# Optimization experiments

Measured on AMD Instinct MI355X. Metric: run time of the kernel, lower is better.

The kernel has to match this reference:

```python
import jax, jax.numpy as jnp
import numpy as np

N_EMBD = 1024
EXPAND = 2
D_INNER = N_EMBD * EXPAND          # 2048
D_STATE = 64
N_HEADS = D_INNER // D_STATE       # 32
HEAD_DIM = D_INNER // N_HEADS      # 64
N_GROUPS = 1
D_CONV = 4
N_LAYERS = 48
BATCH, SEQ = 1, 512
PROJ_SIZE = 2 * D_INNER + N_HEADS + 2 * N_GROUPS * D_STATE  # 4256
EPS = 1e-6


def setup_inputs() -> dict:
    key = jax.random.key(0)
    ks = jax.random.split(key, 6)
    init_std = 0.02
    proj_std = 0.02 / np.sqrt(2 * N_LAYERS)
    return {
        "x": jax.random.normal(ks[0], (BATCH, SEQ, N_EMBD), jnp.float32),
        "norm_scale": jnp.ones((N_EMBD,), jnp.float32),
        "w_in": jax.random.normal(ks[1], (N_EMBD, PROJ_SIZE), jnp.float32) * init_std,
        "conv_weight": jax.random.normal(ks[2], (D_CONV, D_INNER), jnp.float32) * 0.02,
        "conv_bias": jnp.zeros((D_INNER,), jnp.float32),
        "A_log": jnp.log(0.5 + jnp.arange(N_HEADS, dtype=jnp.float32) * 0.5 / N_HEADS),
        "dt_bias": jax.random.normal(ks[3], (N_HEADS,), jnp.float32) * 0.1,
        "w_out": jax.random.normal(ks[4], (D_INNER, N_EMBD), jnp.float32) * proj_std,
    }


def _mamba_fwd(x, norm_scale, w_in, conv_weight, conv_bias, A_log, dt_bias, w_out):
    b, T, _ = x.shape
    residual = x
    # RMSNorm
    xn = x * jax.lax.rsqrt(jnp.mean(x * x, axis=-1, keepdims=True) + EPS) * norm_scale
    # in_proj and split
    proj = xn @ w_in  # (b, T, proj_size)
    gate = proj[..., :D_INNER]
    ssm_in = proj[..., D_INNER:2 * D_INNER]
    dt_raw = proj[..., 2 * D_INNER:2 * D_INNER + N_HEADS]
    gs = N_GROUPS * D_STATE
    B = proj[..., 2 * D_INNER + N_HEADS:2 * D_INNER + N_HEADS + gs].reshape(b, T, N_GROUPS, D_STATE)
    C = proj[..., 2 * D_INNER + N_HEADS + gs:].reshape(b, T, N_GROUPS, D_STATE)
    # causal depthwise short conv (cross-correlation, matching lax.conv semantics)
    xp = jnp.pad(ssm_in, ((0, 0), (D_CONV - 1, 0), (0, 0)))
    conv = conv_bias + sum(conv_weight[k] * xp[:, k:k + T, :] for k in range(D_CONV))
    h = jax.nn.silu(conv)  # (b, T, d_inner)
    dt = jax.nn.softplus(dt_raw + dt_bias)  # (b, T, H)
    A = -jnp.exp(A_log)  # (H,)
    A_bar = jnp.exp(A[None, None, :] * dt)  # (b, T, H)
    # heads / groups
    hpg = N_HEADS // N_GROUPS
    xh = h.reshape(b, T, N_HEADS, HEAD_DIM)
    Bh = jnp.repeat(B, hpg, axis=2)  # (b, T, H, N)
    Ch = jnp.repeat(C, hpg, axis=2)  # (b, T, H, N)
    # Bu[b,t,h,p,n] = B[b,t,h,n] * dt[b,t,h] * x[b,t,h,p]
    Bu = Bh[:, :, :, None, :] * (dt[..., None, None] * xh[..., None])  # (b,T,H,P,N)

    def _binary_op(left, right):
        a_l, b_l = left
        a_r, b_r = right
        return (a_l * a_r, a_r * b_l + b_r)

    # A_bar broadcast to (b,T,H,1,1) so the pair broadcasts against Bu
    _, states = jax.lax.associative_scan(_binary_op, (A_bar[..., None, None], Bu), axis=1)
    y = jnp.einsum('bthpn,bthn->bthp', states, Ch).reshape(b, T, D_INNER)
    y = y * jax.nn.silu(gate)
    y = y @ w_out
    return residual + y


def reference(x, norm_scale, w_in, conv_weight, conv_bias, A_log, dt_bias, w_out):
    return _mamba_fwd(x, norm_scale, w_in, conv_weight, conv_bias, A_log, dt_bias, w_out)
```

## Files before the change

### kernel.cpp

```cpp
#include <hip/hip_runtime.h>
#include <hip/hip_bf16.h>

typedef unsigned short u16;
typedef float f32x4v __attribute__((ext_vector_type(4)));
typedef short short8 __attribute__((ext_vector_type(8)));

#define TSEQ 512
#define EMB  1024
#define DI   2048
#define NH   32
#define DS   64
#define PROJ 4256
#define PROJP 4352
#define NCH  8
#define LCH  64
#define KSPLIT2 4

__device__ __forceinline__ u16 f2bf(float f) {
    union { __hip_bfloat16 h; u16 u; } cv;
    cv.h = __float2bfloat16(f);
    return cv.u;
}
__device__ __forceinline__ unsigned pack2(float a, float b) {
    return (unsigned)f2bf(a) | ((unsigned)f2bf(b) << 16);
}

__global__ __launch_bounds__(256) void k_transpose_cast(
        const float* __restrict__ src, u16* __restrict__ dst, int K, int N) {
    __shared__ float tile[64][65];
    const int n0 = blockIdx.x * 64;
    const int k0 = blockIdx.y * 64;
    const int tid = threadIdx.x;
    const int c  = tid & 63;
    const int r4 = tid >> 6;
    #pragma unroll
    for (int i = 0; i < 16; ++i) {
        int r = r4 + i * 4;
        float v = 0.f;
        if (n0 + c < N) v = src[(size_t)(k0 + r) * N + n0 + c];
        tile[r][c] = v;
    }
    __syncthreads();
    const int rk = tid & 63;
    const int cn = tid >> 6;
    #pragma unroll
    for (int i = 0; i < 16; ++i) {
        int n = cn + i * 4;
        dst[(size_t)(n0 + n) * K + k0 + rk] = f2bf(tile[rk][n]);
    }
}

__global__ __launch_bounds__(256) void k_rmsnorm(
        const float* __restrict__ x, const float* __restrict__ scale,
        u16* __restrict__ xnb) {
    const int t = blockIdx.x, tid = threadIdx.x;
    const float4* xr = (const float4*)(x + (size_t)t * EMB);
    float4 v = xr[tid];
    float ss = v.x * v.x + v.y * v.y + v.z * v.z + v.w * v.w;
    #pragma unroll
    for (int off = 32; off; off >>= 1) ss += __shfl_xor(ss, off);
    __shared__ float ws4[4];
    if ((tid & 63) == 0) ws4[tid >> 6] = ss;
    __syncthreads();
    float tot = ws4[0] + ws4[1] + ws4[2] + ws4[3];
    float inv = rsqrtf(tot * (1.f / EMB) + 1e-6f);
    float4 s = ((const float4*)scale)[tid];
    uint2 o;
    o.x = pack2(v.x * inv * s.x, v.y * inv * s.y);
    o.y = pack2(v.z * inv * s.z, v.w * inv * s.w);
    ((uint2*)xnb)[(size_t)t * 256 + tid] = o;
}

template<int BM, int BN>
__global__ __launch_bounds__(256) void k_gemm(
        const u16* __restrict__ A, int lda,
        const u16* __restrict__ BT, int ldb,
        float* __restrict__ C, int ldc, int Kper) {
    constexpr int WM = BM / 2, WN = BN / 2, FM = WM / 16, FN = WN / 16;
    constexpr int NA = BM * 8 / 256, NB = BN * 8 / 256;
    __shared__ __align__(16) u16 Al[BM][72];
    __shared__ __align__(16) u16 Bl[BN][72];
    const int tid = threadIdx.x;
    const int wid = tid >> 6, lane = tid & 63;
    const int wr = wid >> 1, wc = wid & 1;
    const int ar = lane & 15, kg = lane >> 4;
    const int row0 = blockIdx.y * BM, col0 = blockIdx.x * BN;
    const int kbase = blockIdx.z * Kper;
    const int Mtot = gridDim.y * BM;
    float* Cz = C + (size_t)blockIdx.z * Mtot * ldc;

    short8 ra[NA], rb[NB];
    auto load_stage = [&](int k0) {
        #pragma unroll
        for (int j = 0; j < NA; ++j) {
            int idx = tid + j * 256;
            ra[j] = *(const short8*)(A + (size_t)(row0 + (idx >> 3)) * lda + k0 + (idx & 7) * 8);
        }
        #pragma unroll
        for (int j = 0; j < NB; ++j) {
            int idx = tid + j * 256;
            rb[j] = *(const short8*)(BT + (size_t)(col0 + (idx >> 3)) * ldb + k0 + (idx & 7) * 8);
        }
    };
    auto write_stage = [&]() {
        #pragma unroll
        for (int j = 0; j < NA; ++j) {
            int idx = tid + j * 256;
            *(short8*)&Al[idx >> 3][(idx & 7) * 8] = ra[j];
        }
        #pragma unroll
        for (int j = 0; j < NB; ++j) {
            int idx = tid + j * 256;
            *(short8*)&Bl[idx >> 3][(idx & 7) * 8] = rb[j];
        }
    };

    f32x4v acc[FM][FN] = {};
    const int NT = Kper / 64;
    load_stage(kbase);
    for (int kt = 0; kt < NT; ++kt) {
        write_stage();
        __syncthreads();
        if (kt + 1 < NT) load_stage(kbase + (kt + 1) * 64);
        #pragma unroll
        for (int kk = 0; kk < 2; ++kk) {
            short8 af[FM], bf[FN];
            #pragma unroll
            for (int m = 0; m < FM; ++m)
                af[m] = *(const short8*)&Al[wr * WM + m * 16 + ar][kk * 32 + kg * 8];
            #pragma unroll
            for (int n = 0; n < FN; ++n)
                bf[n] = *(const short8*)&Bl[wc * WN + n * 16 + ar][kk * 32 + kg * 8];
            #pragma unroll
            for (int m = 0; m < FM; ++m)
                #pragma unroll
                for (int n = 0; n < FN; ++n)
                    acc[m][n] = __builtin_amdgcn_mfma_f32_16x16x32_bf16(
                        af[m], bf[n], acc[m][n], 0, 0, 0);
        }
        __syncthreads();
    }
    #pragma unroll
    for (int m = 0; m < FM; ++m)
        #pragma unroll
        for (int n = 0; n < FN; ++n)
            #pragma unroll
            for (int j = 0; j < 4; ++j) {
                int row = row0 + wr * WM + m * 16 + kg * 4 + j;
                int col = col0 + wc * WN + n * 16 + ar;
                Cz[(size_t)row * ldc + col] = acc[m][n][j];
            }
}

__global__ __launch_bounds__(256) void k_reduce_out(
        const float* __restrict__ part, const float* __restrict__ x,
        float* __restrict__ out) {
    int i = blockIdx.x * 256 + threadIdx.x;
    float4 v = ((const float4*)x)[i];
    #pragma unroll
    for (int z = 0; z < KSPLIT2; ++z) {
        float4 p = ((const float4*)part)[(size_t)z * (TSEQ * EMB / 4) + i];
        v.x += p.x; v.y += p.y; v.z += p.z; v.w += p.w;
    }
    ((float4*)out)[i] = v;
}

__global__ __launch_bounds__(256) void k_dt(
        const float* __restrict__ proj, const float* __restrict__ A_log,
        const float* __restrict__ dt_bias, float* __restrict__ dtw,
        float* __restrict__ abw) {
    int idx = blockIdx.x * 256 + threadIdx.x;
    int t = idx >> 5, hh = idx & 31;
    float z = proj[(size_t)t * PROJP + 2 * DI + hh] + dt_bias[hh];
    float dt = (z > 20.f) ? z : log1pf(expf(z));
    float ab = expf(-expf(A_log[hh]) * dt);
    dtw[idx] = dt;
    abw[idx] = ab;
}

__global__ __launch_bounds__(256) void k_conv(
        const float* __restrict__ proj, const float* __restrict__ cw,
        const float* __restrict__ cb, float* __restrict__ hout) {
    int idx = blockIdx.x * 256 + threadIdx.x;
    int t = idx >> 11, c = idx & 2047;
    float acc = cb[c];
    #pragma unroll
    for (int k = 0; k < 4; ++k) {
        int tt = t + k - 3;
        if (tt >= 0) acc += cw[k * DI + c] * proj[(size_t)tt * PROJP + DI + c];
    }
    hout[idx] = acc / (1.f + expf(-acc));
}

__global__ __launch_bounds__(256) void k_scan1(
        const float* __restrict__ proj, const float* __restrict__ hconv,
        const float* __restrict__ dtw, const float* __restrict__ abw,
        float* __restrict__ Sloc, float* __restrict__ Pc) {
    const int c = blockIdx.x, h = blockIdx.y;
    const int tid = threadIdx.x;
    const int q = tid & 3, p = tid >> 2, n0 = q * 16;
    __shared__ __align__(16) float Blds[64][64];
    __shared__ __align__(16) float xl[64][64];
    __shared__ float al[64], dl[64];
    for (int i = tid; i < 4096; i += 256) {
        int t = i >> 6, n = i & 63;
        Blds[t][n] = proj[(size_t)(c * 64 + t) * PROJP + 2 * DI + NH + n];
        xl[t][n]   = hconv[(size_t)(c * 64 + t) * DI + h * 64 + n];
    }
    if (tid < 64) {
        al[tid] = abw[(c * 64 + tid) * NH + h];
        dl[tid] = dtw[(c * 64 + tid) * NH + h];
    }
    __syncthreads();
    float s[16] = {0.f,0.f,0.f,0.f,0.f,0.f,0.f,0.f,0.f,0.f,0.f,0.f,0.f,0.f,0.f,0.f};
    for (int t = 0; t < 64; ++t) {
        float a = al[t];
        float dtx = dl[t] * xl[t][p];
        const float4* brow = (const float4*)&Blds[t][n0];
        #pragma unroll
        for (int i4 = 0; i4 < 4; ++i4) {
            float4 b = brow[i4];
            s[i4*4+0] = a * s[i4*4+0] + dtx * b.x;
            s[i4*4+1] = a * s[i4*4+1] + dtx * b.y;
            s[i4*4+2] = a * s[i4*4+2] + dtx * b.z;
            s[i4*4+3] = a * s[i4*4+3] + dtx * b.w;
        }
    }
    float* dst = Sloc + ((size_t)(c * 32 + h) * 64 + p) * 64 + n0;
    #pragma unroll
    for (int i4 = 0; i4 < 4; ++i4)
        ((float4*)dst)[i4] = make_float4(s[i4*4], s[i4*4+1], s[i4*4+2], s[i4*4+3]);
    if (tid == 0) {
        float pr = 1.f;
        for (int t = 0; t < 64; ++t) pr *= al[t];
        Pc[c * 32 + h] = pr;
    }
}

__global__ __launch_bounds__(256) void k_scan2(
        const float* __restrict__ Sloc, const float* __restrict__ Pc,
        float* __restrict__ Sinit) {
    int gid = blockIdx.x * 256 + threadIdx.x;
    int h = gid >> 12, rem = gid & 4095;
    float s = 0.f;
    #pragma unroll
    for (int c = 0; c < NCH; ++c) {
        size_t o = (size_t)(c * 32 + h) * 4096 + rem;
        Sinit[o] = s;
        s = Pc[c * 32 + h] * s + Sloc[o];
    }
}

__global__ __launch_bounds__(256) void k_scan3(
        const float* __restrict__ proj, const float* __restrict__ hconv,
        const float* __restrict__ dtw, const float* __restrict__ abw,
        const float* __restrict__ Sinit, u16* __restrict__ yg) {
    const int c = blockIdx.x, h = blockIdx.y;
    const int tid = threadIdx.x;
    const int q = tid & 3, p = tid >> 2, n0 = q * 16;
    __shared__ __align__(16) float Blds[64][64];
    __shared__ __align__(16) float Clds[64][64];
    __shared__ __align__(16) float xl[64][64];
    __shared__ float al[64], dl[64];
    for (int i = tid; i < 4096; i += 256) {
        int t = i >> 6, n = i & 63;
        Blds[t][n] = proj[(size_t)(c * 64 + t) * PROJP + 2 * DI + NH + n];
        Clds[t][n] = proj[(size_t)(c * 64 + t) * PROJP + 2 * DI + NH + DS + n];
        xl[t][n]   = hconv[(size_t)(c * 64 + t) * DI + h * 64 + n];
    }
    if (tid < 64) {
        al[tid] = abw[(c * 64 + tid) * NH + h];
        dl[tid] = dtw[(c * 64 + tid) * NH + h];
    }
    __syncthreads();
    float s[16];
    const float* si = Sinit + ((size_t)(c * 32 + h) * 64 + p) * 64 + n0;
    #pragma unroll
    for (int i4 = 0; i4 < 4; ++i4) {
        float4 v = ((const float4*)si)[i4];
        s[i4*4+0] = v.x; s[i4*4+1] = v.y; s[i4*4+2] = v.z; s[i4*4+3] = v.w;
    }
    for (int t = 0; t < 64; ++t) {
        float a = al[t];
        float dtx = dl[t] * xl[t][p];
        const float4* brow = (const float4*)&Blds[t][n0];
        const float4* crow = (const float4*)&Clds[t][n0];
        float yp = 0.f;
        #pragma unroll
        for (int i4 = 0; i4 < 4; ++i4) {
            float4 b = brow[i4], cc = crow[i4];
            s[i4*4+0] = a * s[i4*4+0] + dtx * b.x; yp += s[i4*4+0] * cc.x;
            s[i4*4+1] = a * s[i4*4+1] + dtx * b.y; yp += s[i4*4+1] * cc.y;
            s[i4*4+2] = a * s[i4*4+2] + dtx * b.z; yp += s[i4*4+2] * cc.z;
            s[i4*4+3] = a * s[i4*4+3] + dtx * b.w; yp += s[i4*4+3] * cc.w;
        }
        yp += __shfl_xor(yp, 1);
        yp += __shfl_xor(yp, 2);
        if (q == 0) xl[t][p] = yp;
    }
    __syncthreads();
    for (int i = tid; i < 4096; i += 256) {
        int t = i >> 6, pp = i & 63;
        float y = xl[t][pp];
        float g = proj[(size_t)(c * 64 + t) * PROJP + h * 64 + pp];
        float gy = y * (g / (1.f + expf(-g)));
        yg[(size_t)(c * 64 + t) * DI + h * 64 + pp] = f2bf(gy);
    }
}

extern "C" void kernel_launch(void* const* d_in, const int* in_sizes, int n_in,
                              void* d_out, int out_size, void* d_ws, size_t ws_size,
                              hipStream_t stream) {
    (void)in_sizes; (void)n_in; (void)out_size; (void)ws_size;
    const float* x       = (const float*)d_in[0];
    const float* nscale  = (const float*)d_in[1];
    const float* w_in    = (const float*)d_in[2];
    const float* conv_w  = (const float*)d_in[3];
    const float* conv_b  = (const float*)d_in[4];
    const float* A_log   = (const float*)d_in[5];
    const float* dt_bias = (const float*)d_in[6];
    const float* w_out   = (const float*)d_in[7];
    float* out = (float*)d_out;

    char* wsp = (char*)d_ws;
    auto alloc = [&](size_t bytes) {
        char* ptr = wsp;
        wsp += (bytes + 255) & ~(size_t)255;
        return ptr;
    };
    u16*   w_inT  = (u16*)  alloc((size_t)PROJP * 1024 * 2);
    u16*   w_outT = (u16*)  alloc((size_t)1024 * 2048 * 2);
    u16*   xnb    = (u16*)  alloc((size_t)512 * 1024 * 2);
    float* proj   = (float*)alloc((size_t)512 * PROJP * 4);
    float* hconv  = (float*)alloc((size_t)512 * 2048 * 4);
    float* dtw    = (float*)alloc((size_t)512 * 32 * 4);
    float* abw    = (float*)alloc((size_t)512 * 32 * 4);
    float* Pc     = (float*)alloc((size_t)256 * 4);
    float* Sloc   = (float*)alloc((size_t)NCH * 32 * 4096 * 4);
    float* Sinit  = (float*)alloc((size_t)NCH * 32 * 4096 * 4);
    u16*   yg     = (u16*)  alloc((size_t)512 * 2048 * 2);
    float* part2  = (float*)alloc((size_t)KSPLIT2 * 512 * 1024 * 4);

    k_transpose_cast<<<dim3(68, 16), 256, 0, stream>>>(w_in, w_inT, 1024, PROJ);
    k_transpose_cast<<<dim3(16, 32), 256, 0, stream>>>(w_out, w_outT, 2048, 1024);
    k_rmsnorm<<<512, 256, 0, stream>>>(x, nscale, xnb);
    k_gemm<64, 128><<<dim3(34, 8, 1), 256, 0, stream>>>(
        xnb, 1024, w_inT, 1024, proj, PROJP, 1024);
    k_dt<<<64, 256, 0, stream>>>(proj, A_log, dt_bias, dtw, abw);
    k_conv<<<4096, 256, 0, stream>>>(proj, conv_w, conv_b, hconv);
    k_scan1<<<dim3(NCH, 32), 256, 0, stream>>>(proj, hconv, dtw, abw, Sloc, Pc);
    k_scan2<<<512, 256, 0, stream>>>(Sloc, Pc, Sinit);
    k_scan3<<<dim3(NCH, 32), 256, 0, stream>>>(proj, hconv, dtw, abw, Sinit, yg);
    k_gemm<64, 128><<<dim3(8, 8, KSPLIT2), 256, 0, stream>>>(
        yg, 2048, w_outT, 2048, part2, 1024, 2048 / KSPLIT2);
    k_reduce_out<<<512, 256, 0, stream>>>(part2, x, out);
}
```

Baseline: 167.7 us.

## Fuse conv, dt and inter-chunk scan into scan kernels; merge prep kernels

Merges the two weight-transpose launches and RMSNorm into one k_prep launch. Folds the causal depthwise conv with SiLU and the dt/A_bar computation into both chunked-scan kernels, so the hconv, dtw and abw buffers are no longer written and read back. Drops k_scan2 by having each k_scan3f block combine the preceding chunks' local states itself. This cuts the launch count from 11 to 6 and removes intermediate global traffic, at the cost of computing the conv twice and a serial prefix loop over earlier chunks inside each scan3 block.

```diff
diff --git a/kernel.cpp b/kernel.cpp
--- a/kernel.cpp
+++ b/kernel.cpp
@@ -24,13 +24,11 @@
 __device__ __forceinline__ unsigned pack2(float a, float b) {
     return (unsigned)f2bf(a) | ((unsigned)f2bf(b) << 16);
 }
-
-__global__ __launch_bounds__(256) void k_transpose_cast(
-        const float* __restrict__ src, u16* __restrict__ dst, int K, int N) {
-    __shared__ float tile[64][65];
-    const int n0 = blockIdx.x * 64;
-    const int k0 = blockIdx.y * 64;
-    const int tid = threadIdx.x;
+__device__ __forceinline__ float silu(float v) { return v / (1.f + expf(-v)); }
+
+__device__ __forceinline__ void transpose_tile(
+        const float* __restrict__ src, u16* __restrict__ dst,
+        int K, int N, int n0, int k0, int tid, float tile[64][65]) {
     const int c  = tid & 63;
     const int r4 = tid >> 6;
     #pragma unroll
@@ -50,25 +48,38 @@
     }
 }
 
-__global__ __launch_bounds__(256) void k_rmsnorm(
+__global__ __launch_bounds__(256) void k_prep(
+        const float* __restrict__ w_in, u16* __restrict__ w_inT,
+        const float* __restrict__ w_out, u16* __restrict__ w_outT,
         const float* __restrict__ x, const float* __restrict__ scale,
         u16* __restrict__ xnb) {
-    const int t = blockIdx.x, tid = threadIdx.x;
-    const float4* xr = (const float4*)(x + (size_t)t * EMB);
-    float4 v = xr[tid];
-    float ss = v.x * v.x + v.y * v.y + v.z * v.z + v.w * v.w;
-    #pragma unroll
-    for (int off = 32; off; off >>= 1) ss += __shfl_xor(ss, off);
-    __shared__ float ws4[4];
-    if ((tid & 63) == 0) ws4[tid >> 6] = ss;
-    __syncthreads();
-    float tot = ws4[0] + ws4[1] + ws4[2] + ws4[3];
-    float inv = rsqrtf(tot * (1.f / EMB) + 1e-6f);
-    float4 s = ((const float4*)scale)[tid];
-    uint2 o;
-    o.x = pack2(v.x * inv * s.x, v.y * inv * s.y);
-    o.y = pack2(v.z * inv * s.z, v.w * inv * s.w);
-    ((uint2*)xnb)[(size_t)t * 256 + tid] = o;
+    __shared__ float tile[64][65];
+    const int b = blockIdx.x;
+    const int tid = threadIdx.x;
+    if (b < 1088) {
+        int bx = b % 68, by = b / 68;
+        transpose_tile(w_in, w_inT, 1024, PROJ, bx * 64, by * 64, tid, tile);
+    } else if (b < 1600) {
+        int b2 = b - 1088;
+        int bx = b2 % 16, by = b2 / 16;
+        transpose_tile(w_out, w_outT, 2048, 1024, bx * 64, by * 64, tid, tile);
+    } else {
+        int t = b - 1600;
+        const float4* xr = (const float4*)(x + (size_t)t * EMB);
+        float4 v = xr[tid];
+        float ss = v.x * v.x + v.y * v.y + v.z * v.z + v.w * v.w;
+        #pragma unroll
+        for (int off = 32; off; off >>= 1) ss += __shfl_xor(ss, off);
+        if ((tid & 63) == 0) tile[0][tid >> 6] = ss;
+        __syncthreads();
+        float tot = tile[0][0] + tile[0][1] + tile[0][2] + tile[0][3];
+        float inv = rsqrtf(tot * (1.f / EMB) + 1e-6f);
+        float4 s = ((const float4*)scale)[tid];
+        uint2 o;
+        o.x = pack2(v.x * inv * s.x, v.y * inv * s.y);
+        o.y = pack2(v.z * inv * s.z, v.w * inv * s.w);
+        ((uint2*)xnb)[(size_t)t * 256 + tid] = o;
+    }
 }
 
 template<int BM, int BN>
@@ -165,57 +176,46 @@
     ((float4*)out)[i] = v;
 }
 
-__global__ __launch_bounds__(256) void k_dt(
-        const float* __restrict__ proj, const float* __restrict__ A_log,
-        const float* __restrict__ dt_bias, float* __restrict__ dtw,
-        float* __restrict__ abw) {
-    int idx = blockIdx.x * 256 + threadIdx.x;
-    int t = idx >> 5, hh = idx & 31;
-    float z = proj[(size_t)t * PROJP + 2 * DI + hh] + dt_bias[hh];
-    float dt = (z > 20.f) ? z : log1pf(expf(z));
-    float ab = expf(-expf(A_log[hh]) * dt);
-    dtw[idx] = dt;
-    abw[idx] = ab;
-}
-
-__global__ __launch_bounds__(256) void k_conv(
+__global__ __launch_bounds__(256) void k_scan1f(
         const float* __restrict__ proj, const float* __restrict__ cw,
-        const float* __restrict__ cb, float* __restrict__ hout) {
-    int idx = blockIdx.x * 256 + threadIdx.x;
-    int t = idx >> 11, c = idx & 2047;
-    float acc = cb[c];
-    #pragma unroll
-    for (int k = 0; k < 4; ++k) {
-        int tt = t + k - 3;
-        if (tt >= 0) acc += cw[k * DI + c] * proj[(size_t)tt * PROJP + DI + c];
-    }
-    hout[idx] = acc / (1.f + expf(-acc));
-}
-
-__global__ __launch_bounds__(256) void k_scan1(
-        const float* __restrict__ proj, const float* __restrict__ hconv,
-        const float* __restrict__ dtw, const float* __restrict__ abw,
+        const float* __restrict__ cb, const float* __restrict__ A_log,
+        const float* __restrict__ dt_bias,
         float* __restrict__ Sloc, float* __restrict__ Pc) {
     const int c = blockIdx.x, h = blockIdx.y;
     const int tid = threadIdx.x;
     const int q = tid & 3, p = tid >> 2, n0 = q * 16;
     __shared__ __align__(16) float Blds[64][64];
-    __shared__ __align__(16) float xl[64][64];
+    __shared__ __align__(16) float xt[67][64];
     __shared__ float al[64], dl[64];
     for (int i = tid; i < 4096; i += 256) {
         int t = i >> 6, n = i & 63;
         Blds[t][n] = proj[(size_t)(c * 64 + t) * PROJP + 2 * DI + NH + n];
-        xl[t][n]   = hconv[(size_t)(c * 64 + t) * DI + h * 64 + n];
+    }
+    for (int i = tid; i < 67 * 64; i += 256) {
+        int r = i >> 6, n = i & 63;
+        int tt = c * 64 - 3 + r;
+        xt[r][n] = (tt >= 0) ? proj[(size_t)tt * PROJP + DI + h * 64 + n] : 0.f;
     }
     if (tid < 64) {
-        al[tid] = abw[(c * 64 + tid) * NH + h];
-        dl[tid] = dtw[(c * 64 + tid) * NH + h];
+        float z = proj[(size_t)(c * 64 + tid) * PROJP + 2 * DI + h] + dt_bias[h];
+        float dt = (z > 20.f) ? z : log1pf(expf(z));
+        dl[tid] = dt;
+        al[tid] = expf(-expf(A_log[h]) * dt);
     }
     __syncthreads();
-    float s[16] = {0.f,0.f,0.f,0.f,0.f,0.f,0.f,0.f,0.f,0.f,0.f,0.f,0.f,0.f,0.f,0.f};
+    const int ch = h * 64 + p;
+    const float cw0 = cw[0 * DI + ch], cw1 = cw[1 * DI + ch];
+    const float cw2 = cw[2 * DI + ch], cw3 = cw[3 * DI + ch];
+    const float cbv = cb[ch];
+    float x0 = xt[0][p], x1 = xt[1][p], x2 = xt[2][p];
+    float s[16] = {};
     for (int t = 0; t < 64; ++t) {
+        float x3 = xt[t + 3][p];
+        float cv = cbv + cw0 * x0 + cw1 * x1 + cw2 * x2 + cw3 * x3;
+        x0 = x1; x1 = x2; x2 = x3;
+        float hv = silu(cv);
         float a = al[t];
-        float dtx = dl[t] * xl[t][p];
+        float dtx = dl[t] * hv;
         const float4* brow = (const float4*)&Blds[t][n0];
         #pragma unroll
         for (int i4 = 0; i4 < 4; ++i4) {
@@ -237,52 +237,61 @@
     }
 }
 
-__global__ __launch_bounds__(256) void k_scan2(
+__global__ __launch_bounds__(256) void k_scan3f(
+        const float* __restrict__ proj, const float* __restrict__ cw,
+        const float* __restrict__ cb, const float* __restrict__ A_log,
+        const float* __restrict__ dt_bias,
         const float* __restrict__ Sloc, const float* __restrict__ Pc,
-        float* __restrict__ Sinit) {
-    int gid = blockIdx.x * 256 + threadIdx.x;
-    int h = gid >> 12, rem = gid & 4095;
-    float s = 0.f;
-    #pragma unroll
-    for (int c = 0; c < NCH; ++c) {
-        size_t o = (size_t)(c * 32 + h) * 4096 + rem;
-        Sinit[o] = s;
-        s = Pc[c * 32 + h] * s + Sloc[o];
-    }
-}
-
-__global__ __launch_bounds__(256) void k_scan3(
-        const float* __restrict__ proj, const float* __restrict__ hconv,
-        const float* __restrict__ dtw, const float* __restrict__ abw,
-        const float* __restrict__ Sinit, u16* __restrict__ yg) {
+        u16* __restrict__ yg) {
     const int c = blockIdx.x, h = blockIdx.y;
     const int tid = threadIdx.x;
     const int q = tid & 3, p = tid >> 2, n0 = q * 16;
     __shared__ __align__(16) float Blds[64][64];
     __shared__ __align__(16) float Clds[64][64];
-    __shared__ __align__(16) float xl[64][64];
+    __shared__ __align__(16) float xt[67][64];
     __shared__ float al[64], dl[64];
     for (int i = tid; i < 4096; i += 256) {
         int t = i >> 6, n = i & 63;
         Blds[t][n] = proj[(size_t)(c * 64 + t) * PROJP + 2 * DI + NH + n];
         Clds[t][n] = proj[(size_t)(c * 64 + t) * PROJP + 2 * DI + NH + DS + n];
-        xl[t][n]   = hconv[(size_t)(c * 64 + t) * DI + h * 64 + n];
+    }
+    for (int i = tid; i < 67 * 64; i += 256) {
+        int r = i >> 6, n = i & 63;
+        int tt = c * 64 - 3 + r;
+        xt[r][n] = (tt >= 0) ? proj[(size_t)tt * PROJP + DI + h * 64 + n] : 0.f;
     }
     if (tid < 64) {
-        al[tid] = abw[(c * 64 + tid) * NH + h];
-        dl[tid] = dtw[(c * 64 + tid) * NH + h];
+        float z = proj[(size_t)(c * 64 + tid) * PROJP + 2 * DI + h] + dt_bias[h];
+        float dt = (z > 20.f) ? z : log1pf(expf(z));
+        dl[tid] = dt;
+        al[tid] = expf(-expf(A_log[h]) * dt);
     }
     __syncthreads();
-    float s[16];
-    const float* si = Sinit + ((size_t)(c * 32 + h) * 64 + p) * 64 + n0;
-    #pragma unroll
-    for (int i4 = 0; i4 < 4; ++i4) {
-        float4 v = ((const float4*)si)[i4];
-        s[i4*4+0] = v.x; s[i4*4+1] = v.y; s[i4*4+2] = v.z; s[i4*4+3] = v.w;
-    }
+    float s[16] = {};
+    for (int j = 0; j < c; ++j) {
+        float pcv = Pc[j * 32 + h];
+        const float4* sj = (const float4*)(Sloc + ((size_t)(j * 32 + h) * 64 + p) * 64 + n0);
+        #pragma unroll
+        for (int i4 = 0; i4 < 4; ++i4) {
+            float4 v = sj[i4];
+            s[i4*4+0] = pcv * s[i4*4+0] + v.x;
+            s[i4*4+1] = pcv * s[i4*4+1] + v.y;
+            s[i4*4+2] = pcv * s[i4*4+2] + v.z;
+            s[i4*4+3] = pcv * s[i4*4+3] + v.w;
+        }
+    }
+    const int ch = h * 64 + p;
+    const float cw0 = cw[0 * DI + ch], cw1 = cw[1 * DI + ch];
+    const float cw2 = cw[2 * DI + ch], cw3 = cw[3 * DI + ch];
+    const float cbv = cb[ch];
+    float x0 = xt[0][p], x1 = xt[1][p], x2 = xt[2][p];
     for (int t = 0; t < 64; ++t) {
+        float x3 = xt[t + 3][p];
+        float cv = cbv + cw0 * x0 + cw1 * x1 + cw2 * x2 + cw3 * x3;
+        x0 = x1; x1 = x2; x2 = x3;
+        float hv = silu(cv);
         float a = al[t];
-        float dtx = dl[t] * xl[t][p];
+        float dtx = dl[t] * hv;
         const float4* brow = (const float4*)&Blds[t][n0];
         const float4* crow = (const float4*)&Clds[t][n0];
         float yp = 0.f;
@@ -296,15 +305,14 @@
         }
         yp += __shfl_xor(yp, 1);
         yp += __shfl_xor(yp, 2);
-        if (q == 0) xl[t][p] = yp;
+        if (q == 0) xt[t][p] = yp;
     }
     __syncthreads();
     for (int i = tid; i < 4096; i += 256) {
         int t = i >> 6, pp = i & 63;
-        float y = xl[t][pp];
+        float y = xt[t][pp];
         float g = proj[(size_t)(c * 64 + t) * PROJP + h * 64 + pp];
-        float gy = y * (g / (1.f + expf(-g)));
-        yg[(size_t)(c * 64 + t) * DI + h * 64 + pp] = f2bf(gy);
+        yg[(size_t)(c * 64 + t) * DI + h * 64 + pp] = f2bf(y * silu(g));
     }
 }
 
@@ -332,25 +340,18 @@
     u16*   w_outT = (u16*)  alloc((size_t)1024 * 2048 * 2);
     u16*   xnb    = (u16*)  alloc((size_t)512 * 1024 * 2);
     float* proj   = (float*)alloc((size_t)512 * PROJP * 4);
-    float* hconv  = (float*)alloc((size_t)512 * 2048 * 4);
-    float* dtw    = (float*)alloc((size_t)512 * 32 * 4);
-    float* abw    = (float*)alloc((size_t)512 * 32 * 4);
     float* Pc     = (float*)alloc((size_t)256 * 4);
     float* Sloc   = (float*)alloc((size_t)NCH * 32 * 4096 * 4);
-    float* Sinit  = (float*)alloc((size_t)NCH * 32 * 4096 * 4);
     u16*   yg     = (u16*)  alloc((size_t)512 * 2048 * 2);
     float* part2  = (float*)alloc((size_t)KSPLIT2 * 512 * 1024 * 4);
 
-    k_transpose_cast<<<dim3(68, 16), 256, 0, stream>>>(w_in, w_inT, 1024, PROJ);
-    k_transpose_cast<<<dim3(16, 32), 256, 0, stream>>>(w_out, w_outT, 2048, 1024);
-    k_rmsnorm<<<512, 256, 0, stream>>>(x, nscale, xnb);
+    k_prep<<<2112, 256, 0, stream>>>(w_in, w_inT, w_out, w_outT, x, nscale, xnb);
     k_gemm<64, 128><<<dim3(34, 8, 1), 256, 0, stream>>>(
         xnb, 1024, w_inT, 1024, proj, PROJP, 1024);
-    k_dt<<<64, 256, 0, stream>>>(proj, A_log, dt_bias, dtw, abw);
-    k_conv<<<4096, 256, 0, stream>>>(proj, conv_w, conv_b, hconv);
-    k_scan1<<<dim3(NCH, 32), 256, 0, stream>>>(proj, hconv, dtw, abw, Sloc, Pc);
-    k_scan2<<<512, 256, 0, stream>>>(Sloc, Pc, Sinit);
-    k_scan3<<<dim3(NCH, 32), 256, 0, stream>>>(proj, hconv, dtw, abw, Sinit, yg);
+    k_scan1f<<<dim3(NCH, 32), 256, 0, stream>>>(
+        proj, conv_w, conv_b, A_log, dt_bias, Sloc, Pc);
+    k_scan3f<<<dim3(NCH, 32), 256, 0, stream>>>(
+        proj, conv_w, conv_b, A_log, dt_bias, Sloc, Pc, yg);
     k_gemm<64, 128><<<dim3(8, 8, KSPLIT2), 256, 0, stream>>>(
         yg, 2048, w_outT, 2048, part2, 1024, 2048 / KSPLIT2);
     k_reduce_out<<<512, 256, 0, stream>>>(part2, x, out);
```

New measurement: 170.5 us. About the same (+1.7%).
